# Kernel optimization log

Hardware: AMD Instinct MI355X
Metric: run time of the kernel (lower is better)

The kernel has to match this reference:

```python
import jax, jax.numpy as jnp
import numpy as np

B, T, C = 4, 2048, 1024
H, HS = 16, 64  # n_heads, head_size; H*HS == C


def setup_inputs() -> dict:
    key = jax.random.key(0)
    ks = jax.random.split(key, 6)
    s = 0.02
    x = jax.random.normal(ks[0], (B, T, C), dtype=jnp.float32)
    Wq = jax.random.normal(ks[1], (H, C, HS), dtype=jnp.float32) * s
    Wk = jax.random.normal(ks[2], (H, C, HS), dtype=jnp.float32) * s
    Wv = jax.random.normal(ks[3], (H, C, HS), dtype=jnp.float32) * s
    Wo = jax.random.normal(ks[4], (C, C), dtype=jnp.float32) * s
    bo = jnp.zeros((C,), dtype=jnp.float32)
    return {"x": x, "Wq": Wq, "Wk": Wk, "Wv": Wv, "Wo": Wo, "bo": bo}


def reference(x, Wq, Wk, Wv, Wo, bo):
    # batched multi-head causal attention (math identical to per-head loop)
    q = jnp.einsum('btc,hcd->bhtd', x, Wq)  # [B,H,T,HS]
    k = jnp.einsum('btc,hcd->bhtd', x, Wk)
    v = jnp.einsum('btc,hcd->bhtd', x, Wv)
    scale = 1.0 / jnp.sqrt(jnp.asarray(HS, x.dtype))
    scores = jnp.einsum('bhtd,bhsd->bhts', q, k) * scale  # [B,H,T,T]
    causal = jnp.tril(jnp.ones((T, T), dtype=bool))
    scores = jnp.where(causal, scores, jnp.asarray(-jnp.inf, scores.dtype))
    attn = jax.nn.softmax(scores, axis=-1)
    out = jnp.einsum('bhts,bhsd->bhtd', attn, v)  # [B,H,T,HS]
    # concat heads along feature dim (head order == module list order)
    out = out.transpose(0, 2, 1, 3).reshape(B, T, C)
    return out @ Wo.T + bo
```

## Files before the change

### kernel.cpp

```cpp
#include <hip/hip_runtime.h>

typedef __attribute__((ext_vector_type(8))) short v8s;
typedef __attribute__((ext_vector_type(4))) short v4s;
typedef __attribute__((ext_vector_type(4))) float v4f;

static __device__ __forceinline__ short f2bf(float f) {
  union { float f; unsigned u; } c; c.f = f;
  unsigned r = c.u + 0x7fffu + ((c.u >> 16) & 1u);
  return (short)(r >> 16);
}

static __device__ __forceinline__ unsigned pk_bf16(float a, float b) {
  union { float f; unsigned u; } ca, cb; ca.f = a; cb.f = b;
  return ((ca.u + 0x8000u) >> 16) | ((cb.u + 0x8000u) & 0xffff0000u);
}

#if __has_builtin(__builtin_amdgcn_exp2f)
#define EXP2(x) __builtin_amdgcn_exp2f(x)
#else
#define EXP2(x) exp2f(x)
#endif

#define GLDS(gp, lp) __builtin_amdgcn_global_load_lds( \
    (const __attribute__((address_space(1))) void*)(gp), \
    (__attribute__((address_space(3))) void*)(lp), 16, 0, 0)


__global__ __launch_bounds__(256) void cast_f32_bf16(const float* __restrict__ src,
                                                     short* __restrict__ dst) {
  int idx = (blockIdx.x * 256 + threadIdx.x) * 4;
  float4 v = *(const float4*)(src + idx);
  v4s o; o.x = f2bf(v.x); o.y = f2bf(v.y); o.z = f2bf(v.z); o.w = f2bf(v.w);
  *(v4s*)(dst + idx) = o;
}

__global__ __launch_bounds__(256) void build_wt(const float* __restrict__ Wq,
                                                const float* __restrict__ Wk,
                                                const float* __restrict__ Wv,
                                                short* __restrict__ Wt) {
  __shared__ float tile[64][65];
  int blk = blockIdx.x;
  int sel = blk >> 8, rest = blk & 255;
  int h = rest >> 4, kt = rest & 15;
  const float* W = (sel == 0) ? Wq : ((sel == 1) ? Wk : Wv);
  int k0 = kt * 64;
  int tid = threadIdx.x;
  for (int i = 0; i < 4; ++i) {
    int c = i * 256 + tid;
    int row = c >> 4, c4 = (c & 15) * 4;
    float4 v = *(const float4*)(W + (size_t)h * 65536 + (size_t)(k0 + row) * 64 + c4);
    tile[row][c4 + 0] = v.x; tile[row][c4 + 1] = v.y;
    tile[row][c4 + 2] = v.z; tile[row][c4 + 3] = v.w;
  }
  __syncthreads();
  for (int i = 0; i < 2; ++i) {
    int c = i * 256 + tid;
    int d = c >> 3, k8 = (c & 7) * 8;
    v8s o;
    for (int j = 0; j < 8; ++j) o[j] = f2bf(tile[k8 + j][d]);
    *(v8s*)(Wt + (size_t)(sel * 1024 + h * 64 + d) * 1024 + k0 + k8) = o;
  }
}

__global__ __launch_bounds__(256) void transpose_v(const short* __restrict__ V,
                                                   short* __restrict__ Vt) {
  __shared__ short tile[64][72];
  int bh = blockIdx.x >> 5, tt = blockIdx.x & 31;
  int t0 = tt * 64;
  int tid = threadIdx.x;
  for (int i = 0; i < 2; ++i) {
    int c = i * 256 + tid;
    int row = c >> 3, col8 = (c & 7) * 8;
    v8s v = *(const v8s*)(V + ((size_t)(bh * 2048 + t0 + row)) * 64 + col8);
    *(v8s*)&tile[row][col8] = v;
  }
  __syncthreads();
  for (int i = 0; i < 2; ++i) {
    int c = i * 256 + tid;
    int d = c >> 3, t8 = (c & 7) * 8;
    v8s o;
    for (int j = 0; j < 8; ++j) o[j] = tile[t8 + j][d];
    *(v8s*)(Vt + ((size_t)(bh * 64 + d)) * 2048 + t0 + t8) = o;
  }
}


__global__ __launch_bounds__(256) void gemm_qkv(const short* __restrict__ Xb,
                                                const short* __restrict__ Wt,
                                                short* __restrict__ Qo,
                                                short* __restrict__ Ko,
                                                short* __restrict__ Vo) {
  __shared__ short lA[128 * 32];
  __shared__ short lB[128 * 32];
  const int tid = threadIdx.x;
  const int lane = tid & 63, quad = lane >> 4, l16 = lane & 15;
  const int wave = tid >> 6;
  const int m0 = blockIdx.x * 128, n0 = blockIdx.y * 128;
  const int wm = (wave >> 1) * 64, wn = (wave & 1) * 64;
  v4f acc[4][4];
  for (int i = 0; i < 4; ++i)
    for (int j = 0; j < 4; ++j) acc[i][j] = (v4f){0.f, 0.f, 0.f, 0.f};

  for (int k0 = 0; k0 < 1024; k0 += 32) {
    __syncthreads();
    for (int i = 0; i < 2; ++i) {
      int c = i * 256 + tid;
      int row = c >> 2, kc = c & 3;
      GLDS(Xb + (size_t)(m0 + row) * 1024 + k0 + kc * 8, lA + c * 8);
      GLDS(Wt + (size_t)(n0 + row) * 1024 + k0 + kc * 8, lB + c * 8);
    }
    __syncthreads();
    v8s a[4], b[4];
    for (int mt = 0; mt < 4; ++mt) a[mt] = *(const v8s*)&lA[(wm + mt * 16 + l16) * 32 + quad * 8];
    for (int nt = 0; nt < 4; ++nt) b[nt] = *(const v8s*)&lB[(wn + nt * 16 + l16) * 32 + quad * 8];
    for (int mt = 0; mt < 4; ++mt)
      for (int nt = 0; nt < 4; ++nt)
        acc[mt][nt] = __builtin_amdgcn_mfma_f32_16x16x32_bf16(a[mt], b[nt], acc[mt][nt], 0, 0, 0);
  }

  int selu = n0 >> 10;
  short* obase = (selu == 0) ? Qo : ((selu == 1) ? Ko : Vo);
  for (int nt = 0; nt < 4; ++nt) {
    int n = n0 + wn + nt * 16 + l16;
    int hd = n & 1023;
    int h = hd >> 6, d = hd & 63;
    for (int mt = 0; mt < 4; ++mt)
      for (int r = 0; r < 4; ++r) {
        int m = m0 + wm + mt * 16 + quad * 4 + r;
        int b_ = m >> 11, t = m & 2047;
        obase[(size_t)((b_ * 16 + h) * 2048 + t) * 64 + d] = f2bf(acc[mt][nt][r]);
      }
  }
}


__global__ __launch_bounds__(256, 2) void attn(const short* __restrict__ Q,
                                               const short* __restrict__ K,
                                               const short* __restrict__ Vt,
                                               short* __restrict__ AO) {
  __shared__ short lK[64 * 64];
  __shared__ short lV[64 * 64];
  __shared__ short lP[4 * 32 * 72];
  const int tid = threadIdx.x;
  const int w = tid >> 6, lane = tid & 63, quad = lane >> 4, l16 = lane & 15;
  const int bh = blockIdx.x & 63, pr = blockIdx.x >> 6;
  const float kexp = 0.18033688011112042f;
  const unsigned psel = 0x07060302u;
  short* pw = lP + w * (32 * 72);
  const size_t qkbase = (size_t)bh * 2048 * 64;
  const size_t vtbase = (size_t)bh * 64 * 2048;
  const int b_ = bh >> 4, h = bh & 15;

  const int r0 = tid >> 3, cp = tid & 7;
  const int cl0 = cp ^ (r0 & 7);
  const int r1 = r0 + 32;
  const int cl1 = cp ^ (r1 & 7);

  const int swz = l16 & 7;
  const int ph0 = (quad ^ swz) * 8;
  const int ph1 = ((quad + 4) ^ swz) * 8;

  for (int phase = 0; phase < 2; ++phase) {
    const int c = phase ? (15 - pr) : pr;
    const int qc = c * 128 + w * 32;

    v8s bQ[2][2];
#pragma unroll
    for (int qs = 0; qs < 2; ++qs) {
      const short* qb = Q + qkbase + (size_t)(qc + qs * 16 + l16) * 64 + quad * 8;
      bQ[qs][0] = *(const v8s*)(qb);
      bQ[qs][1] = *(const v8s*)(qb + 32);
    }
    v4f accO[2][4];
#pragma unroll
    for (int qs = 0; qs < 2; ++qs)
      for (int g = 0; g < 4; ++g) accO[qs][g] = (v4f){0.f, 0.f, 0.f, 0.f};
    float lrun[2] = {0.f, 0.f};

    const int nst = 2 * c + 2;
    for (int kt = 0; kt < nst; ++kt) {
      const int kb = kt * 64;
      __syncthreads();
      GLDS(K + qkbase + (size_t)(kb + r0) * 64 + cl0 * 8, lK + tid * 8);
      GLDS(K + qkbase + (size_t)(kb + r1) * 64 + cl1 * 8, lK + tid * 8 + 2048);
      GLDS(Vt + vtbase + (size_t)r0 * 2048 + kb + cl0 * 8, lV + tid * 8);
      GLDS(Vt + vtbase + (size_t)r1 * 2048 + kb + cl1 * 8, lV + tid * 8 + 2048);
      __syncthreads();

      const bool act0 = kb < qc + 16;
      const bool act1 = kb < qc + 32;
      if (!act1) continue;

      v8s aK[4][2];
#pragma unroll
      for (int mt = 0; mt < 4; ++mt) {
        const short* kr = lK + (mt * 16 + l16) * 64;
        aK[mt][0] = *(const v8s*)(kr + ph0);
        aK[mt][1] = *(const v8s*)(kr + ph1);
      }
#pragma unroll
      for (int qs = 0; qs < 2; ++qs) {
        if (qs == 0 ? !act0 : false) continue;
        const int rbase = qc + qs * 16;
        v4f sT[4];
#pragma unroll
        for (int mt = 0; mt < 4; ++mt) {
          v4f t = (v4f){0.f, 0.f, 0.f, 0.f};
          t = __builtin_amdgcn_mfma_f32_16x16x32_bf16(aK[mt][0], bQ[qs][0], t, 0, 0, 0);
          t = __builtin_amdgcn_mfma_f32_16x16x32_bf16(aK[mt][1], bQ[qs][1], t, 0, 0, 0);
          sT[mt] = t;
        }
        if (kb + 63 >= rbase) {
          const int kq = kb + quad * 4 - (rbase + l16);
#pragma unroll
          for (int mt = 0; mt < 4; ++mt)
#pragma unroll
            for (int r = 0; r < 4; ++r)
              if (kq + mt * 16 + r > 0) sT[mt][r] = -__builtin_inff();
        }
        float ls = lrun[qs];
#pragma unroll
        for (int mt = 0; mt < 4; ++mt) {
          float p0 = EXP2(sT[mt][0] * kexp);
          float p1 = EXP2(sT[mt][1] * kexp);
          float p2 = EXP2(sT[mt][2] * kexp);
          float p3 = EXP2(sT[mt][3] * kexp);
          ls += (p0 + p1) + (p2 + p3);
          int2 dw;
          dw.x = (int)__builtin_amdgcn_perm(__float_as_uint(p1), __float_as_uint(p0), psel);
          dw.y = (int)__builtin_amdgcn_perm(__float_as_uint(p3), __float_as_uint(p2), psel);
          *(int2*)&pw[(qs * 16 + l16) * 72 + mt * 16 + quad * 4] = dw;
        }
        lrun[qs] = ls;
      }
      v8s aV[4][2];
#pragma unroll
      for (int g = 0; g < 4; ++g) {
        const short* vr = lV + (g * 16 + l16) * 64;
        aV[g][0] = *(const v8s*)(vr + ph0);
        aV[g][1] = *(const v8s*)(vr + ph1);
      }
#pragma unroll
      for (int qs = 0; qs < 2; ++qs) {
        if (qs == 0 ? !act0 : false) continue;
        v8s bP0 = *(const v8s*)&pw[(qs * 16 + l16) * 72 + quad * 8];
        v8s bP1 = *(const v8s*)&pw[(qs * 16 + l16) * 72 + 32 + quad * 8];
#pragma unroll
        for (int g = 0; g < 4; ++g) {
          accO[qs][g] = __builtin_amdgcn_mfma_f32_16x16x32_bf16(aV[g][0], bP0, accO[qs][g], 0, 0, 0);
          accO[qs][g] = __builtin_amdgcn_mfma_f32_16x16x32_bf16(aV[g][1], bP1, accO[qs][g], 0, 0, 0);
        }
      }
    }

#pragma unroll
    for (int qs = 0; qs < 2; ++qs) {
      float ls = lrun[qs];
      ls += __shfl_xor(ls, 16);
      ls += __shfl_xor(ls, 32);
      float inv = __builtin_amdgcn_rcpf(ls);
      int t = qc + qs * 16 + l16;
      short* ao = AO + ((size_t)(b_ * 2048 + t)) * 1024 + h * 64 + quad * 4;
#pragma unroll
      for (int g = 0; g < 4; ++g) {
        int2 dw;
        dw.x = (int)pk_bf16(accO[qs][g][0] * inv, accO[qs][g][1] * inv);
        dw.y = (int)pk_bf16(accO[qs][g][2] * inv, accO[qs][g][3] * inv);
        *(int2*)(ao + g * 16) = dw;
      }
    }
  }
}


__global__ __launch_bounds__(256) void gemm_out(const short* __restrict__ AO,
                                                const short* __restrict__ Wot,
                                                const float* __restrict__ bo,
                                                float* __restrict__ out) {
  __shared__ short lA[128 * 32];
  __shared__ short lB[128 * 32];
  const int tid = threadIdx.x;
  const int lane = tid & 63, quad = lane >> 4, l16 = lane & 15;
  const int wave = tid >> 6;
  const int m0 = blockIdx.x * 128, n0 = blockIdx.y * 128;
  const int wm = (wave >> 1) * 64, wn = (wave & 1) * 64;
  v4f acc[4][4];
  for (int i = 0; i < 4; ++i)
    for (int j = 0; j < 4; ++j) acc[i][j] = (v4f){0.f, 0.f, 0.f, 0.f};

  for (int k0 = 0; k0 < 1024; k0 += 32) {
    __syncthreads();
    for (int i = 0; i < 2; ++i) {
      int c = i * 256 + tid;
      int row = c >> 2, kc = c & 3;
      GLDS(AO + (size_t)(m0 + row) * 1024 + k0 + kc * 8, lA + c * 8);
      GLDS(Wot + (size_t)(n0 + row) * 1024 + k0 + kc * 8, lB + c * 8);
    }
    __syncthreads();
    v8s a[4], b[4];
    for (int mt = 0; mt < 4; ++mt) a[mt] = *(const v8s*)&lA[(wm + mt * 16 + l16) * 32 + quad * 8];
    for (int nt = 0; nt < 4; ++nt) b[nt] = *(const v8s*)&lB[(wn + nt * 16 + l16) * 32 + quad * 8];
    for (int mt = 0; mt < 4; ++mt)
      for (int nt = 0; nt < 4; ++nt)
        acc[mt][nt] = __builtin_amdgcn_mfma_f32_16x16x32_bf16(a[mt], b[nt], acc[mt][nt], 0, 0, 0);
  }

  for (int nt = 0; nt < 4; ++nt) {
    int n = n0 + wn + nt * 16 + l16;
    float bias = bo[n];
    for (int mt = 0; mt < 4; ++mt)
      for (int r = 0; r < 4; ++r) {
        int m = m0 + wm + mt * 16 + quad * 4 + r;
        out[(size_t)m * 1024 + n] = acc[mt][nt][r] + bias;
      }
  }
}


extern "C" void kernel_launch(void* const* d_in, const int* in_sizes, int n_in,
                              void* d_out, int out_size, void* d_ws, size_t ws_size,
                              hipStream_t stream) {
  const float* x  = (const float*)d_in[0];
  const float* Wq = (const float*)d_in[1];
  const float* Wk = (const float*)d_in[2];
  const float* Wv = (const float*)d_in[3];
  const float* Wo = (const float*)d_in[4];
  const float* bo = (const float*)d_in[5];
  float* out = (float*)d_out;
  char* ws = (char*)d_ws;

  short* Xb  = (short*)(ws);
  short* Wt  = (short*)(ws + (16u << 20));
  short* Wot = (short*)(ws + (22u << 20));
  short* Q   = (short*)(ws + (24u << 20));
  short* K   = (short*)(ws + (40u << 20));
  short* V   = (short*)(ws + (56u << 20));
  short* Vt  = (short*)(ws + (72u << 20));

  cast_f32_bf16<<<8192, 256, 0, stream>>>(x, Xb);
  cast_f32_bf16<<<1024, 256, 0, stream>>>(Wo, Wot);
  build_wt<<<768, 256, 0, stream>>>(Wq, Wk, Wv, Wt);
  gemm_qkv<<<dim3(64, 24), 256, 0, stream>>>(Xb, Wt, Q, K, V);
  transpose_v<<<2048, 256, 0, stream>>>(V, Vt);
  attn<<<dim3(512), 256, 0, stream>>>(Q, K, Vt, Xb);
  gemm_out<<<dim3(64, 8), 256, 0, stream>>>(Xb, Wot, bo, out);
}
```

Before: 245.3 us.

## Pipeline QKV GEMM with 4-stage LDS ring and write V transposed directly

Rewrites the QKV projection GEMM to use 512-thread blocks over 256x128 tiles. A 4-deep ring of LDS buffers is filled by async global-to-LDS loads issued three k-steps ahead, with XOR-swizzled LDS offsets and s_setprio around the MFMA bursts. The epilogue writes the V output directly in transposed layout with packed bf16 stores, which removes the separate transpose_v kernel and its extra round trip through memory. In exchange it uses more LDS per block, which may lower occupancy, and the V stores become strided 8-byte writes.

```diff
diff --git a/kernel.cpp b/kernel.cpp
--- a/kernel.cpp
+++ b/kernel.cpp
@@ -62,74 +62,120 @@
   }
 }
 
-__global__ __launch_bounds__(256) void transpose_v(const short* __restrict__ V,
-                                                   short* __restrict__ Vt) {
-  __shared__ short tile[64][72];
-  int bh = blockIdx.x >> 5, tt = blockIdx.x & 31;
-  int t0 = tt * 64;
-  int tid = threadIdx.x;
-  for (int i = 0; i < 2; ++i) {
-    int c = i * 256 + tid;
-    int row = c >> 3, col8 = (c & 7) * 8;
-    v8s v = *(const v8s*)(V + ((size_t)(bh * 2048 + t0 + row)) * 64 + col8);
-    *(v8s*)&tile[row][col8] = v;
-  }
-  __syncthreads();
-  for (int i = 0; i < 2; ++i) {
-    int c = i * 256 + tid;
-    int d = c >> 3, t8 = (c & 7) * 8;
-    v8s o;
-    for (int j = 0; j < 8; ++j) o[j] = tile[t8 + j][d];
-    *(v8s*)(Vt + ((size_t)(bh * 64 + d)) * 2048 + t0 + t8) = o;
-  }
-}
-
-
-__global__ __launch_bounds__(256) void gemm_qkv(const short* __restrict__ Xb,
+
+__global__ __launch_bounds__(512) void gemm_qkv(const short* __restrict__ Xb,
                                                 const short* __restrict__ Wt,
                                                 short* __restrict__ Qo,
                                                 short* __restrict__ Ko,
-                                                short* __restrict__ Vo) {
-  __shared__ short lA[128 * 32];
-  __shared__ short lB[128 * 32];
+                                                short* __restrict__ Vt) {
+  __shared__ short lds[49152];
   const int tid = threadIdx.x;
   const int lane = tid & 63, quad = lane >> 4, l16 = lane & 15;
   const int wave = tid >> 6;
-  const int m0 = blockIdx.x * 128, n0 = blockIdx.y * 128;
+  const int m0 = blockIdx.x * 256, n0 = blockIdx.y * 128;
   const int wm = (wave >> 1) * 64, wn = (wave & 1) * 64;
+
+  const int r0 = tid >> 2, cbs = (tid & 3) ^ ((r0 >> 1) & 3);
+  const size_t offA0 = (size_t)(m0 + r0) * 1024 + cbs * 8;
+  const size_t offB0 = (size_t)(n0 + r0) * 1024 + cbs * 8;
+
+  int aoff[4], boff[4];
+#pragma unroll
+  for (int mt = 0; mt < 4; ++mt) {
+    int row = wm + mt * 16 + l16;
+    aoff[mt] = row * 32 + (quad ^ ((row >> 1) & 3)) * 8;
+  }
+#pragma unroll
+  for (int nt = 0; nt < 4; ++nt) {
+    int row = wn + nt * 16 + l16;
+    boff[nt] = row * 32 + (quad ^ ((row >> 1) & 3)) * 8;
+  }
+
   v4f acc[4][4];
+#pragma unroll
   for (int i = 0; i < 4; ++i)
+#pragma unroll
     for (int j = 0; j < 4; ++j) acc[i][j] = (v4f){0.f, 0.f, 0.f, 0.f};
 
-  for (int k0 = 0; k0 < 1024; k0 += 32) {
-    __syncthreads();
-    for (int i = 0; i < 2; ++i) {
-      int c = i * 256 + tid;
-      int row = c >> 2, kc = c & 3;
-      GLDS(Xb + (size_t)(m0 + row) * 1024 + k0 + kc * 8, lA + c * 8);
-      GLDS(Wt + (size_t)(n0 + row) * 1024 + k0 + kc * 8, lB + c * 8);
-    }
-    __syncthreads();
-    v8s a[4], b[4];
-    for (int mt = 0; mt < 4; ++mt) a[mt] = *(const v8s*)&lA[(wm + mt * 16 + l16) * 32 + quad * 8];
-    for (int nt = 0; nt < 4; ++nt) b[nt] = *(const v8s*)&lB[(wn + nt * 16 + l16) * 32 + quad * 8];
-    for (int mt = 0; mt < 4; ++mt)
-      for (int nt = 0; nt < 4; ++nt)
-        acc[mt][nt] = __builtin_amdgcn_mfma_f32_16x16x32_bf16(a[mt], b[nt], acc[mt][nt], 0, 0, 0);
-  }
-
-  int selu = n0 >> 10;
-  short* obase = (selu == 0) ? Qo : ((selu == 1) ? Ko : Vo);
-  for (int nt = 0; nt < 4; ++nt) {
-    int n = n0 + wn + nt * 16 + l16;
-    int hd = n & 1023;
-    int h = hd >> 6, d = hd & 63;
-    for (int mt = 0; mt < 4; ++mt)
-      for (int r = 0; r < 4; ++r) {
-        int m = m0 + wm + mt * 16 + quad * 4 + r;
-        int b_ = m >> 11, t = m & 2047;
-        obase[(size_t)((b_ * 16 + h) * 2048 + t) * 64 + d] = f2bf(acc[mt][nt][r]);
-      }
+#pragma unroll
+  for (int t = 0; t < 3; ++t) {
+    GLDS(Xb + offA0 + t * 32, lds + t * 8192 + tid * 8);
+    GLDS(Xb + offA0 + 131072 + t * 32, lds + t * 8192 + 4096 + tid * 8);
+    GLDS(Wt + offB0 + t * 32, lds + 32768 + t * 4096 + tid * 8);
+  }
+  asm volatile("s_waitcnt vmcnt(6)" ::: "memory");
+  __builtin_amdgcn_s_barrier();
+
+#pragma unroll 4
+  for (int t = 0; t < 32; ++t) {
+    const int p = t & 3;
+    int tn = t + 3; if (tn > 31) tn = 31;
+    const int pn = (t + 3) & 3;
+    const short* lAp = lds + p * 8192;
+    const short* lBp = lds + 32768 + p * 4096;
+
+    GLDS(Xb + offA0 + tn * 32, lds + pn * 8192 + tid * 8);
+    GLDS(Xb + offA0 + 131072 + tn * 32, lds + pn * 8192 + 4096 + tid * 8);
+    v8s a[4], b[2];
+#pragma unroll
+    for (int mt = 0; mt < 4; ++mt) a[mt] = *(const v8s*)(lAp + aoff[mt]);
+    b[0] = *(const v8s*)(lBp + boff[0]);
+    b[1] = *(const v8s*)(lBp + boff[1]);
+    __builtin_amdgcn_s_setprio(1);
+#pragma unroll
+    for (int mt = 0; mt < 4; ++mt) {
+      acc[mt][0] = __builtin_amdgcn_mfma_f32_16x16x32_bf16(a[mt], b[0], acc[mt][0], 0, 0, 0);
+      acc[mt][1] = __builtin_amdgcn_mfma_f32_16x16x32_bf16(a[mt], b[1], acc[mt][1], 0, 0, 0);
+    }
+    __builtin_amdgcn_s_setprio(0);
+
+    GLDS(Wt + offB0 + tn * 32, lds + 32768 + pn * 4096 + tid * 8);
+    b[0] = *(const v8s*)(lBp + boff[2]);
+    b[1] = *(const v8s*)(lBp + boff[3]);
+    __builtin_amdgcn_s_setprio(1);
+#pragma unroll
+    for (int mt = 0; mt < 4; ++mt) {
+      acc[mt][2] = __builtin_amdgcn_mfma_f32_16x16x32_bf16(a[mt], b[0], acc[mt][2], 0, 0, 0);
+      acc[mt][3] = __builtin_amdgcn_mfma_f32_16x16x32_bf16(a[mt], b[1], acc[mt][3], 0, 0, 0);
+    }
+    __builtin_amdgcn_s_setprio(0);
+
+    asm volatile("s_waitcnt vmcnt(6) lgkmcnt(0)" ::: "memory");
+    __builtin_amdgcn_s_barrier();
+  }
+
+  const int selu = n0 >> 10;
+  if (selu < 2) {
+    short* obase = (selu == 0) ? Qo : Ko;
+#pragma unroll
+    for (int nt = 0; nt < 4; ++nt) {
+      int n = (n0 + wn + nt * 16 + l16) & 1023;
+      int h = n >> 6, d = n & 63;
+#pragma unroll
+      for (int mt = 0; mt < 4; ++mt) {
+        int m = m0 + wm + mt * 16 + quad * 4;
+        int b_ = m >> 11, tt = m & 2047;
+        size_t base = (size_t)((b_ * 16 + h) * 2048 + tt) * 64 + d;
+#pragma unroll
+        for (int r = 0; r < 4; ++r)
+          obase[base + (size_t)r * 64] = f2bf(acc[mt][nt][r]);
+      }
+    }
+  } else {
+#pragma unroll
+    for (int nt = 0; nt < 4; ++nt) {
+      int n = (n0 + wn + nt * 16 + l16) & 1023;
+      int h = n >> 6, d = n & 63;
+#pragma unroll
+      for (int mt = 0; mt < 4; ++mt) {
+        int m = m0 + wm + mt * 16 + quad * 4;
+        int b_ = m >> 11, tt = m & 2047;
+        int2 dw;
+        dw.x = (int)pk_bf16(acc[mt][nt][0], acc[mt][nt][1]);
+        dw.y = (int)pk_bf16(acc[mt][nt][2], acc[mt][nt][3]);
+        *(int2*)(Vt + ((size_t)(b_ * 16 + h) * 64 + d) * 2048 + tt) = dw;
+      }
+    }
   }
 }
 
@@ -334,14 +380,12 @@
   short* Wot = (short*)(ws + (22u << 20));
   short* Q   = (short*)(ws + (24u << 20));
   short* K   = (short*)(ws + (40u << 20));
-  short* V   = (short*)(ws + (56u << 20));
-  short* Vt  = (short*)(ws + (72u << 20));
+  short* Vt  = (short*)(ws + (56u << 20));
 
   cast_f32_bf16<<<8192, 256, 0, stream>>>(x, Xb);
   cast_f32_bf16<<<1024, 256, 0, stream>>>(Wo, Wot);
   build_wt<<<768, 256, 0, stream>>>(Wq, Wk, Wv, Wt);
-  gemm_qkv<<<dim3(64, 24), 256, 0, stream>>>(Xb, Wt, Q, K, V);
-  transpose_v<<<2048, 256, 0, stream>>>(V, Vt);
+  gemm_qkv<<<dim3(32, 24), 512, 0, stream>>>(Xb, Wt, Q, K, Vt);
   attn<<<dim3(512), 256, 0, stream>>>(Q, K, Vt, Xb);
   gemm_out<<<dim3(64, 8), 256, 0, stream>>>(Xb, Wot, bo, out);
 }
```

Result: no change. 243.0 us (-1.0%).
